# Optimization experiments

Hardware: AMD Instinct MI355X
Metric: run time of the kernel (lower is better)

Reference implementation:

```python
import jax, jax.numpy as jnp
import numpy as np

N_NODES = 64
N_EDGES = N_NODES * (N_NODES - 1)  # 4032 (fully connected, no self-loops)
BATCH = 64
N_IN = 64
N_HID = 128
N_OUT = 16


def _linear_params(key, fan_in, fan_out):
    # mimic torch nn.Linear default init: U(-1/sqrt(fan_in), 1/sqrt(fan_in))
    kw, kb = jax.random.split(key)
    s = 1.0 / np.sqrt(fan_in)
    W = jax.random.uniform(kw, (fan_in, fan_out), minval=-s, maxval=s, dtype=jnp.float32)
    b = jax.random.uniform(kb, (fan_out,), minval=-s, maxval=s, dtype=jnp.float32)
    return W, b


def setup_inputs() -> dict:
    key = jax.random.key(0)
    ks = jax.random.split(key, 10)
    # one-hot relation matrices for fully-connected graph without self loops
    pairs = np.array([(i, j) for i in range(N_NODES) for j in range(N_NODES) if i != j])
    eye = np.eye(N_NODES, dtype=np.float32)
    rel_send = jnp.asarray(eye[pairs[:, 0]])  # [E, N]
    rel_rec = jnp.asarray(eye[pairs[:, 1]])   # [E, N]

    x = jax.random.normal(ks[0], (BATCH, N_NODES, N_IN), dtype=jnp.float32)

    w1a, b1a = _linear_params(ks[1], N_IN, N_HID)
    w1b, b1b = _linear_params(ks[2], N_HID, N_HID)
    w2a, b2a = _linear_params(ks[3], 2 * N_HID, N_HID)
    w2b, b2b = _linear_params(ks[4], N_HID, N_HID)
    w3a, b3a = _linear_params(ks[5], N_HID, N_HID)
    w3b, b3b = _linear_params(ks[6], N_HID, N_HID)
    w4a, b4a = _linear_params(ks[7], 3 * N_HID, N_HID)  # factor=True
    w4b, b4b = _linear_params(ks[8], N_HID, N_HID)
    wout, bout = _linear_params(ks[9], N_HID, N_OUT)

    return dict(x=x, rel_rec=rel_rec, rel_send=rel_send,
                w1a=w1a, b1a=b1a, w1b=w1b, b1b=b1b,
                w2a=w2a, b2a=b2a, w2b=w2b, b2b=b2b,
                w3a=w3a, b3a=b3a, w3b=w3b, b3b=b3b,
                w4a=w4a, b4a=b4a, w4b=w4b, b4b=b4b,
                wout=wout, bout=bout)


def _mlp(x, wa, ba, wb, bb):
    # Linear -> ReLU -> Linear
    return jax.nn.relu(x @ wa + ba) @ wb + bb


def reference(x, rel_rec, rel_send,
              w1a, b1a, w1b, b1b,
              w2a, b2a, w2b, b2b,
              w3a, b3a, w3b, b3b,
              w4a, b4a, w4b, b4b,
              wout, bout):
    def node2edge(h):
        receivers = jnp.einsum('en,bnh->beh', rel_rec, h)
        senders = jnp.einsum('en,bnh->beh', rel_send, h)
        return jnp.concatenate([senders, receivers], axis=-1)  # [B,E,2H]

    def edge2node(e):
        agg = jnp.einsum('en,beh->bnh', rel_rec, e)
        norm = rel_rec.sum(0)[None, :, None]  # [1,N,1]
        return agg / (norm + 1e-6)

    h = _mlp(x, w1a, b1a, w1b, b1b)            # [B,N,H]
    e = _mlp(node2edge(h), w2a, b2a, w2b, b2b)  # [B,E,H]
    x_skip = e
    # factor=True branch
    n = _mlp(edge2node(e), w3a, b3a, w3b, b3b)  # [B,N,H]
    e2 = node2edge(n)                           # [B,E,2H]
    e2 = jnp.concatenate([e2, x_skip], axis=2)  # [B,E,3H]
    e2 = _mlp(e2, w4a, b4a, w4b, b4b)           # [B,E,H]
    return e2 @ wout + bout                     # [B,E,n_out]
```

## Files before the change

### kernel.cpp

```cpp
#include <hip/hip_runtime.h>
#include <hip/hip_bf16.h>


#define DI __device__ __forceinline__

typedef short bf16x8 __attribute__((ext_vector_type(8)));
typedef float f32x4 __attribute__((ext_vector_type(4)));
typedef unsigned short u16;
typedef unsigned long long u64;

static constexpr int NN = 64, NE = 4032, H = 128;

DI u16 f2bf(float f) {
  union { float f; unsigned u; } v; v.f = f;
  unsigned u = v.u;
  return (u16)((u + 0x7fffu + ((u >> 16) & 1u)) >> 16);
}
DI unsigned pk2(float a, float b) {
  union { __hip_bfloat162 h; unsigned u; } c;
  c.h = __float22bfloat162_rn(float2{a, b});
  return c.u;
}
DI f32x4 mf(bf16x8 a, bf16x8 b, f32x4 c) {
  return __builtin_amdgcn_mfma_f32_16x16x32_bf16(a, b, c, 0, 0, 0);
}
DI bf16x8 ldfrag(const u16* __restrict__ p, int idx, int l) {
  return *reinterpret_cast<const bf16x8*>(p + (idx * 64 + l) * 8);
}

__global__ __launch_bounds__(64) void prepack_kernel(
    const float* __restrict__ w1a, const float* __restrict__ w1b,
    const float* __restrict__ w2a, const float* __restrict__ w2b,
    const float* __restrict__ w3a, const float* __restrict__ w3b,
    const float* __restrict__ w4a, const float* __restrict__ w4b,
    const float* __restrict__ wout,
    const float* __restrict__ b2b, const float* __restrict__ b4b,
    const float* __restrict__ bout,
    u16* __restrict__ pk, float* __restrict__ c2, float* __restrict__ c4) {
  int seg = blockIdx.y, f = blockIdx.x, l = threadIdx.x;
  int h = l >> 4, mm = l & 15;
  if (seg == 10) {
    if (f >= 4) return;
    union { u16 u[8]; uint4 q; } o;
#pragma unroll
    for (int jj = 0; jj < 8; jj++) {
      int row = f * 32 + h * 8 + jj;
      float s0 = 0.f, s1 = 0.f, s2 = 0.f, s3 = 0.f;
      for (int j = 0; j < 128; j += 4) {
        s0 += w4b[row * 128 + j]     * wout[j * 16 + mm];
        s1 += w4b[row * 128 + j + 1] * wout[(j + 1) * 16 + mm];
        s2 += w4b[row * 128 + j + 2] * wout[(j + 2) * 16 + mm];
        s3 += w4b[row * 128 + j + 3] * wout[(j + 3) * 16 + mm];
      }
      o.u[jj] = f2bf((s0 + s1) + (s2 + s3));
    }
    *reinterpret_cast<uint4*>(pk + ((304 + f) * 64 + l) * 8) = o.q;
    return;
  }
  if (seg == 11) {
    if (f < 2) {
      int o = f * 64 + l;
      float s0 = 0.f, s1 = 0.f;
      for (int k = 0; k < 128; k += 2) {
        s0 += b2b[k] * w4a[(256 + k) * 128 + o];
        s1 += b2b[k + 1] * w4a[(256 + k + 1) * 128 + o];
      }
      c2[o] = s0 + s1;
    } else if (f == 2 && l < 16) {
      float s = bout[l];
      for (int k = 0; k < 128; k++) s += b4b[k] * wout[k * 16 + l];
      c4[l] = s;
    }
    return;
  }
  const float* src; int foff, nfrag, roff, pi;
  switch (seg) {
    case 0:  src = w1a; foff = 0;   nfrag = 16; roff = 0;   pi = 0; break;
    case 1:  src = w1b; foff = 16;  nfrag = 32; roff = 0;   pi = 1; break;
    case 2:  src = w2a; foff = 48;  nfrag = 32; roff = 0;   pi = 1; break;
    case 3:  src = w2a; foff = 80;  nfrag = 32; roff = 128; pi = 1; break;
    case 4:  src = w2b; foff = 112; nfrag = 32; roff = 0;   pi = 0; break;
    case 5:  src = w3a; foff = 144; nfrag = 32; roff = 0;   pi = 1; break;
    case 6:  src = w3b; foff = 176; nfrag = 32; roff = 0;   pi = 1; break;
    case 7:  src = w4a; foff = 208; nfrag = 32; roff = 0;   pi = 1; break;
    case 8:  src = w4a; foff = 240; nfrag = 32; roff = 128; pi = 1; break;
    default: src = w4a; foff = 272; nfrag = 32; roff = 256; pi = 0; break;
  }
  if (f >= nfrag) return;
  int kt = f >> 3, ct = f & 7;
  union { u16 u[8]; uint4 q; } o;
#pragma unroll
  for (int jj = 0; jj < 8; jj++) {
    int row = pi ? (kt * 32 + (jj >> 2) * 16 + h * 4 + (jj & 3))
                 : (kt * 32 + h * 8 + jj);
    o.u[jj] = f2bf(src[(roff + row) * 128 + ct * 16 + mm]);
  }
  *reinterpret_cast<uint4*>(pk + ((foff + f) * 64 + l) * 8) = o.q;
}

__global__ __launch_bounds__(512, 2) void node_kernel(
    const float* __restrict__ x, const u16* __restrict__ pk,
    const float* __restrict__ b1a, const float* __restrict__ b1b,
    const float* __restrict__ b2a,
    float* __restrict__ sproj, float* __restrict__ rproj) {
  __shared__ bf16x8 act[2][4][64];
  int blk = blockIdx.x, b = blk >> 2, nq = blk & 3;
  int tid = threadIdx.x, l = tid & 63, w = tid >> 6;
  int m = l & 15, h = l >> 4;
  int node = nq * 16 + m;
  const f32x4 Z = {0.f, 0.f, 0.f, 0.f};
  bf16x8 wpre[14];
  wpre[0] = ldfrag(pk, w, l);
  wpre[1] = ldfrag(pk, 8 + w, l);
#pragma unroll
  for (int kt = 0; kt < 4; kt++) {
    wpre[2 + kt]  = ldfrag(pk + 16 * 512, kt * 8 + w, l);
    wpre[6 + kt]  = ldfrag(pk + 48 * 512, kt * 8 + w, l);
    wpre[10 + kt] = ldfrag(pk + 80 * 512, kt * 8 + w, l);
  }
  f32x4 acc;
  {
    const float* xb = x + (b * NN + node) * 64;
    bf16x8 xin[2];
#pragma unroll
    for (int kt = 0; kt < 2; kt++) {
      f32x4 a0 = *(const f32x4*)(xb + kt * 32 + h * 8);
      f32x4 a1 = *(const f32x4*)(xb + kt * 32 + h * 8 + 4);
      union { unsigned u[4]; bf16x8 v; } t;
      t.u[0] = pk2(a0[0], a0[1]); t.u[1] = pk2(a0[2], a0[3]);
      t.u[2] = pk2(a1[0], a1[1]); t.u[3] = pk2(a1[2], a1[3]);
      xin[kt] = t.v;
    }
    acc = mf(wpre[0], xin[0], Z);
    acc = mf(wpre[1], xin[1], acc);
    f32x4 bb = *(const f32x4*)(b1a + w * 16 + h * 4);
    union { unsigned u[2]; u64 d; } p;
    p.u[0] = pk2(fmaxf(acc[0] + bb[0], 0.f), fmaxf(acc[1] + bb[1], 0.f));
    p.u[1] = pk2(fmaxf(acc[2] + bb[2], 0.f), fmaxf(acc[3] + bb[3], 0.f));
    reinterpret_cast<u64*>(&act[0][w >> 1][l])[w & 1] = p.d;
  }
  __syncthreads();
  bf16x8 ef[4];
#pragma unroll
  for (int kt = 0; kt < 4; kt++) ef[kt] = act[0][kt][l];
#pragma unroll
  for (int kt = 0; kt < 4; kt++)
    acc = mf(wpre[2 + kt], ef[kt], kt == 0 ? Z : acc);
  {
    f32x4 bb = *(const f32x4*)(b1b + w * 16 + h * 4);
    union { unsigned u[2]; u64 d; } p;
    p.u[0] = pk2(acc[0] + bb[0], acc[1] + bb[1]);
    p.u[1] = pk2(acc[2] + bb[2], acc[3] + bb[3]);
    reinterpret_cast<u64*>(&act[1][w >> 1][l])[w & 1] = p.d;
  }
  __syncthreads();
#pragma unroll
  for (int kt = 0; kt < 4; kt++) ef[kt] = act[1][kt][l];
#pragma unroll
  for (int kt = 0; kt < 4; kt++)
    acc = mf(wpre[6 + kt], ef[kt], kt == 0 ? Z : acc);
  *reinterpret_cast<f32x4*>(sproj + (b * NN + node) * H + w * 16 + h * 4) = acc;
#pragma unroll
  for (int kt = 0; kt < 4; kt++)
    acc = mf(wpre[10 + kt], ef[kt], kt == 0 ? Z : acc);
  {
    f32x4 bb = *(const f32x4*)(b2a + w * 16 + h * 4);
    f32x4 o = acc;
    o[0] += bb[0]; o[1] += bb[1]; o[2] += bb[2]; o[3] += bb[3];
    *reinterpret_cast<f32x4*>(rproj + (b * NN + node) * H + w * 16 + h * 4) = o;
  }
}

__global__ __launch_bounds__(512, 2) void agg_kernel(
    const float* __restrict__ sproj, const float* __restrict__ rproj,
    const u16* __restrict__ pk,
    const float* __restrict__ b2b, const float* __restrict__ b3a,
    const float* __restrict__ b3b, const float* __restrict__ b4a,
    const float* __restrict__ c2,
    float* __restrict__ s4, float* __restrict__ r4) {
  __shared__ f32x4 lred[8][8][64];
  __shared__ bf16x8 act[2][4][64];
  int blk = blockIdx.x, b = blk >> 2, jq = blk & 3;
  int tid = threadIdx.x, l = tid & 63, w = tid >> 6, m = l & 15, h = l >> 4;
  int j = jq * 16 + m;
  const float* rpb = rproj + (b * NN + j) * H;
  f32x4 rpv[8], accS[8];
#pragma unroll
  for (int k = 0; k < 8; k++) {
    rpv[k] = *(const f32x4*)(rpb + (k >> 1) * 32 + h * 8 + (k & 1) * 4);
    accS[k] = f32x4{0.f, 0.f, 0.f, 0.f};
  }
  const float* spb = sproj + b * NN * H;
  for (int i = w * 8; i < w * 8 + 8; i++) {
    const float* sp = spb + i * H;
#pragma unroll
    for (int k = 0; k < 8; k++) {
      f32x4 s = *(const f32x4*)(sp + (k >> 1) * 32 + h * 8 + (k & 1) * 4);
      f32x4 t = s + rpv[k];
      t[0] = fmaxf(t[0], 0.f); t[1] = fmaxf(t[1], 0.f);
      t[2] = fmaxf(t[2], 0.f); t[3] = fmaxf(t[3], 0.f);
      accS[k] += t;
    }
  }
  if ((j >> 3) == w) {
    const float* sp = spb + j * H;
#pragma unroll
    for (int k = 0; k < 8; k++) {
      f32x4 s = *(const f32x4*)(sp + (k >> 1) * 32 + h * 8 + (k & 1) * 4);
      f32x4 t = s + rpv[k];
      accS[k][0] -= fmaxf(t[0], 0.f); accS[k][1] -= fmaxf(t[1], 0.f);
      accS[k][2] -= fmaxf(t[2], 0.f); accS[k][3] -= fmaxf(t[3], 0.f);
    }
  }
#pragma unroll
  for (int k = 0; k < 8; k++) lred[w][k][l] = accS[k];
  bf16x8 wpre[20];
#pragma unroll
  for (int kt = 0; kt < 4; kt++) {
    wpre[kt]      = ldfrag(pk + 112 * 512, kt * 8 + w, l);
    wpre[4 + kt]  = ldfrag(pk + 144 * 512, kt * 8 + w, l);
    wpre[8 + kt]  = ldfrag(pk + 176 * 512, kt * 8 + w, l);
    wpre[12 + kt] = ldfrag(pk + 208 * 512, kt * 8 + w, l);
    wpre[16 + kt] = ldfrag(pk + 240 * 512, kt * 8 + w, l);
  }
  __syncthreads();
  if (w < 4) {
    f32x4 s0 = f32x4{0.f, 0.f, 0.f, 0.f}, s1 = s0;
#pragma unroll
    for (int ww = 0; ww < 8; ww++) {
      s0 += lred[ww][2 * w][l];
      s1 += lred[ww][2 * w + 1][l];
    }
    union { unsigned u[4]; bf16x8 v; } t;
    t.u[0] = pk2(s0[0], s0[1]); t.u[1] = pk2(s0[2], s0[3]);
    t.u[2] = pk2(s1[0], s1[1]); t.u[3] = pk2(s1[2], s1[3]);
    act[0][w][l] = t.v;
  }
  __syncthreads();
  const f32x4 Z = {0.f, 0.f, 0.f, 0.f};
  f32x4 acc;
  bf16x8 ef[4];
#pragma unroll
  for (int kt = 0; kt < 4; kt++) ef[kt] = act[0][kt][l];
#pragma unroll
  for (int kt = 0; kt < 4; kt++)
    acc = mf(wpre[kt], ef[kt], kt == 0 ? Z : acc);
  {
    const float inv = 1.0f / (63.0f + 1e-6f);
    const float binv = 63.0f * inv;
    f32x4 bb = *(const f32x4*)(b2b + w * 16 + h * 4);
    union { unsigned u[2]; u64 d; } p;
    p.u[0] = pk2(acc[0] * inv + bb[0] * binv, acc[1] * inv + bb[1] * binv);
    p.u[1] = pk2(acc[2] * inv + bb[2] * binv, acc[3] * inv + bb[3] * binv);
    reinterpret_cast<u64*>(&act[1][w >> 1][l])[w & 1] = p.d;
  }
  __syncthreads();
#pragma unroll
  for (int kt = 0; kt < 4; kt++) ef[kt] = act[1][kt][l];
#pragma unroll
  for (int kt = 0; kt < 4; kt++)
    acc = mf(wpre[4 + kt], ef[kt], kt == 0 ? Z : acc);
  {
    f32x4 bb = *(const f32x4*)(b3a + w * 16 + h * 4);
    union { unsigned u[2]; u64 d; } p;
    p.u[0] = pk2(fmaxf(acc[0] + bb[0], 0.f), fmaxf(acc[1] + bb[1], 0.f));
    p.u[1] = pk2(fmaxf(acc[2] + bb[2], 0.f), fmaxf(acc[3] + bb[3], 0.f));
    reinterpret_cast<u64*>(&act[0][w >> 1][l])[w & 1] = p.d;
  }
  __syncthreads();
#pragma unroll
  for (int kt = 0; kt < 4; kt++) ef[kt] = act[0][kt][l];
#pragma unroll
  for (int kt = 0; kt < 4; kt++)
    acc = mf(wpre[8 + kt], ef[kt], kt == 0 ? Z : acc);
  {
    f32x4 bb = *(const f32x4*)(b3b + w * 16 + h * 4);
    union { unsigned u[2]; u64 d; } p;
    p.u[0] = pk2(acc[0] + bb[0], acc[1] + bb[1]);
    p.u[1] = pk2(acc[2] + bb[2], acc[3] + bb[3]);
    reinterpret_cast<u64*>(&act[1][w >> 1][l])[w & 1] = p.d;
  }
  __syncthreads();
#pragma unroll
  for (int kt = 0; kt < 4; kt++) ef[kt] = act[1][kt][l];
#pragma unroll
  for (int kt = 0; kt < 4; kt++)
    acc = mf(wpre[12 + kt], ef[kt], kt == 0 ? Z : acc);
  {
    f32x4 cc = *(const f32x4*)(c2 + w * 16 + h * 4);
    f32x4 o = acc;
    o[0] += cc[0]; o[1] += cc[1]; o[2] += cc[2]; o[3] += cc[3];
    *reinterpret_cast<f32x4*>(s4 + (b * NN + j) * H + w * 16 + h * 4) = o;
  }
#pragma unroll
  for (int kt = 0; kt < 4; kt++)
    acc = mf(wpre[16 + kt], ef[kt], kt == 0 ? Z : acc);
  {
    f32x4 bb = *(const f32x4*)(b4a + w * 16 + h * 4);
    f32x4 o = acc;
    o[0] += bb[0]; o[1] += bb[1]; o[2] += bb[2]; o[3] += bb[3];
    *reinterpret_cast<f32x4*>(r4 + (b * NN + j) * H + w * 16 + h * 4) = o;
  }
}

__global__ __launch_bounds__(256, 4) void edge_kernel(
    const float* __restrict__ sproj, const float* __restrict__ rproj,
    const float* __restrict__ s4, const float* __restrict__ r4,
    const u16* __restrict__ pk, const float* __restrict__ c4,
    float* __restrict__ out) {
  __shared__ alignas(16) u16 bufA[8192];
  __shared__ alignas(16) u16 bufB[8192];
  int blk = blockIdx.x;
  int wg = (blk & 7) * 512 + (blk >> 3);
  int b = wg >> 6, i = wg & 63;
  int tid = threadIdx.x, l = tid & 63, w = tid >> 6;
  int m16 = l & 15, h = l >> 4;
  const f32x4 Z = {0.f, 0.f, 0.f, 0.f};
  int jnv[4];
#pragma unroll
  for (int n = 0; n < 4; n++) {
    int e = n * 16 + m16;
    int v = e + (e >= i ? 1 : 0); jnv[n] = v > 63 ? 63 : v;
  }
  bf16x8 wfv[4];
#pragma unroll
  for (int kt = 0; kt < 4; kt++) wfv[kt] = ldfrag(pk + 304 * 512, kt, l);
  f32x4 c4v = *(const f32x4*)(c4 + h * 4);
  {
    const float* spp = sproj + (b * NN + i) * H + w * 32 + h * 8;
    f32x4 s0 = *(const f32x4*)spp, s1 = *(const f32x4*)(spp + 4);
#pragma unroll
    for (int n = 0; n < 4; n++) {
      const float* rpp = rproj + (b * NN + jnv[n]) * H + w * 32 + h * 8;
      f32x4 r0 = *(const f32x4*)rpp, r1 = *(const f32x4*)(rpp + 4);
      union { unsigned u[4]; uint4 q; } t;
      t.u[0] = pk2(fmaxf(s0[0] + r0[0], 0.f), fmaxf(s0[1] + r0[1], 0.f));
      t.u[1] = pk2(fmaxf(s0[2] + r0[2], 0.f), fmaxf(s0[3] + r0[3], 0.f));
      t.u[2] = pk2(fmaxf(s1[0] + r1[0], 0.f), fmaxf(s1[1] + r1[1], 0.f));
      t.u[3] = pk2(fmaxf(s1[2] + r1[2], 0.f), fmaxf(s1[3] + r1[3], 0.f));
      *reinterpret_cast<uint4*>(&bufA[((w * 4 + n) * 64 + l) * 8]) = t.q;
    }
  }
  bf16x8 wv[8];
#pragma unroll
  for (int idx = 0; idx < 8; idx++)
    wv[idx] = ldfrag(pk + 112 * 512, (idx >> 1) * 8 + 2 * w + (idx & 1), l);
  __syncthreads();
  f32x4 acc[2][4];
  __builtin_amdgcn_s_setprio(1);
#pragma unroll
  for (int n = 0; n < 4; n++) {
    bf16x8 bf[4];
#pragma unroll
    for (int kt = 0; kt < 4; kt++)
      bf[kt] = *reinterpret_cast<const bf16x8*>(&bufA[((kt * 4 + n) * 64 + l) * 8]);
#pragma unroll
    for (int kt = 0; kt < 4; kt++)
#pragma unroll
      for (int m = 0; m < 2; m++)
        acc[m][n] = mf(wv[kt * 2 + m], bf[kt], kt == 0 ? Z : acc[m][n]);
  }
  __builtin_amdgcn_s_setprio(0);
#pragma unroll
  for (int idx = 0; idx < 8; idx++)
    wv[idx] = ldfrag(pk + 272 * 512, (idx >> 1) * 8 + 2 * w + (idx & 1), l);
  {
    int lane2b = (h >> 1) * 16 + m16;
    int jb = (h & 1) * 4;
#pragma unroll
    for (int m = 0; m < 2; m++)
#pragma unroll
      for (int n = 0; n < 4; n++) {
        union { unsigned u[2]; u64 d; } p;
        p.u[0] = pk2(acc[m][n][0], acc[m][n][1]);
        p.u[1] = pk2(acc[m][n][2], acc[m][n][3]);
        *reinterpret_cast<u64*>(
            &bufB[((w * 4 + n) * 64 + lane2b + m * 32) * 8 + jb]) = p.d;
      }
  }
  f32x4 s4v[2], rv[4][2];
#pragma unroll
  for (int m = 0; m < 2; m++)
    s4v[m] = *(const f32x4*)(s4 + (b * NN + i) * H + w * 32 + m * 16 + h * 4);
#pragma unroll
  for (int n = 0; n < 4; n++) {
    const float* r4p = r4 + (b * NN + jnv[n]) * H + w * 32 + h * 4;
#pragma unroll
    for (int m = 0; m < 2; m++) rv[n][m] = *(const f32x4*)(r4p + m * 16);
  }
  __syncthreads();
  __builtin_amdgcn_s_setprio(1);
#pragma unroll
  for (int n = 0; n < 4; n++) {
    bf16x8 bf[4];
#pragma unroll
    for (int kt = 0; kt < 4; kt++)
      bf[kt] = *reinterpret_cast<const bf16x8*>(&bufB[((kt * 4 + n) * 64 + l) * 8]);
#pragma unroll
    for (int kt = 0; kt < 4; kt++)
#pragma unroll
      for (int m = 0; m < 2; m++)
        acc[m][n] = mf(wv[kt * 2 + m], bf[kt], kt == 0 ? Z : acc[m][n]);
  }
  __builtin_amdgcn_s_setprio(0);
  {
    int lane2b = (h >> 1) * 16 + m16;
    int jb = (h & 1) * 4;
#pragma unroll
    for (int n = 0; n < 4; n++)
#pragma unroll
      for (int m = 0; m < 2; m++) {
        f32x4 r = rv[n][m];
        union { unsigned u[2]; u64 d; } p;
        p.u[0] = pk2(fmaxf(acc[m][n][0] + s4v[m][0] + r[0], 0.f),
                     fmaxf(acc[m][n][1] + s4v[m][1] + r[1], 0.f));
        p.u[1] = pk2(fmaxf(acc[m][n][2] + s4v[m][2] + r[2], 0.f),
                     fmaxf(acc[m][n][3] + s4v[m][3] + r[3], 0.f));
        *reinterpret_cast<u64*>(
            &bufA[((w * 4 + n) * 64 + lane2b + m * 32) * 8 + jb]) = p.d;
      }
  }
  __syncthreads();
  {
    bf16x8 bf[4];
#pragma unroll
    for (int kt = 0; kt < 4; kt++)
      bf[kt] = *reinterpret_cast<const bf16x8*>(&bufA[((kt * 4 + w) * 64 + l) * 8]);
    f32x4 a4 = Z;
#pragma unroll
    for (int kt = 0; kt < 4; kt++) a4 = mf(wfv[kt], bf[kt], a4);
    int jj = w * 16 + m16;
    if (jj < 63) {
      f32x4 o;
      o[0] = a4[0] + c4v[0]; o[1] = a4[1] + c4v[1];
      o[2] = a4[2] + c4v[2]; o[3] = a4[3] + c4v[3];
      *reinterpret_cast<f32x4*>(out + (b * NE + i * 63 + jj) * 16 + h * 4) = o;
    }
  }
}

extern "C" void kernel_launch(void* const* d_in, const int* in_sizes, int n_in,
                              void* d_out, int out_size, void* d_ws, size_t ws_size,
                              hipStream_t stream) {
  const float* x    = (const float*)d_in[0];
  const float* w1a  = (const float*)d_in[3];
  const float* b1a  = (const float*)d_in[4];
  const float* w1b  = (const float*)d_in[5];
  const float* b1b  = (const float*)d_in[6];
  const float* w2a  = (const float*)d_in[7];
  const float* b2a  = (const float*)d_in[8];
  const float* w2b  = (const float*)d_in[9];
  const float* b2b  = (const float*)d_in[10];
  const float* w3a  = (const float*)d_in[11];
  const float* b3a  = (const float*)d_in[12];
  const float* w3b  = (const float*)d_in[13];
  const float* b3b  = (const float*)d_in[14];
  const float* w4a  = (const float*)d_in[15];
  const float* b4a  = (const float*)d_in[16];
  const float* w4b  = (const float*)d_in[17];
  const float* b4b  = (const float*)d_in[18];
  const float* wout = (const float*)d_in[19];
  const float* bout = (const float*)d_in[20];
  float* out = (float*)d_out;

  float* sproj = (float*)d_ws;
  float* rproj = sproj + 524288;
  float* s4    = rproj + 524288;
  float* r4    = s4 + 524288;
  u16* pkw     = (u16*)(r4 + 524288);
  float* c2    = (float*)(pkw + 174080);
  float* c4    = c2 + 128;

  prepack_kernel<<<dim3(32, 12), 64, 0, stream>>>(
      w1a, w1b, w2a, w2b, w3a, w3b, w4a, w4b, wout, b2b, b4b, bout, pkw, c2, c4);
  node_kernel<<<256, 512, 0, stream>>>(x, pkw, b1a, b1b, b2a, sproj, rproj);
  agg_kernel<<<256, 512, 0, stream>>>(sproj, rproj, pkw, b2b, b3a, b3b, b4a, c2, s4, r4);
  edge_kernel<<<4096, 256, 0, stream>>>(sproj, rproj, s4, r4, pkw, c4, out);
}
```

Measured before the change: 94.77 us.

## Split edge kernel work across 8 waves per block instead of 4

```diff
diff --git a/kernel.cpp b/kernel.cpp
--- a/kernel.cpp
+++ b/kernel.cpp
@@ -303,7 +303,7 @@
   }
 }
 
-__global__ __launch_bounds__(256, 4) void edge_kernel(
+__global__ __launch_bounds__(512, 6) void edge_kernel(
     const float* __restrict__ sproj, const float* __restrict__ rproj,
     const float* __restrict__ s4, const float* __restrict__ r4,
     const u16* __restrict__ pk, const float* __restrict__ c4,
@@ -313,128 +313,97 @@
   int blk = blockIdx.x;
   int wg = (blk & 7) * 512 + (blk >> 3);
   int b = wg >> 6, i = wg & 63;
-  int tid = threadIdx.x, l = tid & 63, w = tid >> 6;
+  int tid = threadIdx.x, l = tid & 63, w8 = tid >> 6;
+  int n = w8 & 3, fh = w8 >> 2;
   int m16 = l & 15, h = l >> 4;
   const f32x4 Z = {0.f, 0.f, 0.f, 0.f};
-  int jnv[4];
-#pragma unroll
-  for (int n = 0; n < 4; n++) {
-    int e = n * 16 + m16;
-    int v = e + (e >= i ? 1 : 0); jnv[n] = v > 63 ? 63 : v;
-  }
-  bf16x8 wfv[4];
-#pragma unroll
-  for (int kt = 0; kt < 4; kt++) wfv[kt] = ldfrag(pk + 304 * 512, kt, l);
-  f32x4 c4v = *(const f32x4*)(c4 + h * 4);
-  {
-    const float* spp = sproj + (b * NN + i) * H + w * 32 + h * 8;
-    f32x4 s0 = *(const f32x4*)spp, s1 = *(const f32x4*)(spp + 4);
-#pragma unroll
-    for (int n = 0; n < 4; n++) {
-      const float* rpp = rproj + (b * NN + jnv[n]) * H + w * 32 + h * 8;
-      f32x4 r0 = *(const f32x4*)rpp, r1 = *(const f32x4*)(rpp + 4);
+  int e = n * 16 + m16;
+  int jn = e + (e >= i ? 1 : 0); if (jn > 63) jn = 63;
+  {
+    const float* sp = sproj + (b * NN + i) * H;
+    const float* rp = rproj + (b * NN + jn) * H;
+#pragma unroll
+    for (int kk = 0; kk < 2; kk++) {
+      int kt = fh * 2 + kk;
+      int k0 = kt * 32 + h * 8;
+      f32x4 s0 = *(const f32x4*)(sp + k0), s1 = *(const f32x4*)(sp + k0 + 4);
+      f32x4 r0 = *(const f32x4*)(rp + k0), r1 = *(const f32x4*)(rp + k0 + 4);
       union { unsigned u[4]; uint4 q; } t;
       t.u[0] = pk2(fmaxf(s0[0] + r0[0], 0.f), fmaxf(s0[1] + r0[1], 0.f));
       t.u[1] = pk2(fmaxf(s0[2] + r0[2], 0.f), fmaxf(s0[3] + r0[3], 0.f));
       t.u[2] = pk2(fmaxf(s1[0] + r1[0], 0.f), fmaxf(s1[1] + r1[1], 0.f));
       t.u[3] = pk2(fmaxf(s1[2] + r1[2], 0.f), fmaxf(s1[3] + r1[3], 0.f));
-      *reinterpret_cast<uint4*>(&bufA[((w * 4 + n) * 64 + l) * 8]) = t.q;
-    }
-  }
-  bf16x8 wv[8];
-#pragma unroll
-  for (int idx = 0; idx < 8; idx++)
-    wv[idx] = ldfrag(pk + 112 * 512, (idx >> 1) * 8 + 2 * w + (idx & 1), l);
-  __syncthreads();
-  f32x4 acc[2][4];
+      *reinterpret_cast<uint4*>(&bufA[((kt * 4 + n) * 64 + l) * 8]) = t.q;
+    }
+  }
+  __syncthreads();
+  f32x4 acc[4];
   __builtin_amdgcn_s_setprio(1);
 #pragma unroll
-  for (int n = 0; n < 4; n++) {
-    bf16x8 bf[4];
-#pragma unroll
-    for (int kt = 0; kt < 4; kt++)
-      bf[kt] = *reinterpret_cast<const bf16x8*>(&bufA[((kt * 4 + n) * 64 + l) * 8]);
-#pragma unroll
-    for (int kt = 0; kt < 4; kt++)
-#pragma unroll
-      for (int m = 0; m < 2; m++)
-        acc[m][n] = mf(wv[kt * 2 + m], bf[kt], kt == 0 ? Z : acc[m][n]);
+  for (int kt = 0; kt < 4; kt++) {
+    bf16x8 bf = *reinterpret_cast<const bf16x8*>(&bufA[((kt * 4 + n) * 64 + l) * 8]);
+#pragma unroll
+    for (int c = 0; c < 4; c++) {
+      bf16x8 wv = ldfrag(pk + 112 * 512, kt * 8 + fh * 4 + c, l);
+      acc[c] = mf(wv, bf, kt == 0 ? Z : acc[c]);
+    }
   }
   __builtin_amdgcn_s_setprio(0);
 #pragma unroll
-  for (int idx = 0; idx < 8; idx++)
-    wv[idx] = ldfrag(pk + 272 * 512, (idx >> 1) * 8 + 2 * w + (idx & 1), l);
-  {
-    int lane2b = (h >> 1) * 16 + m16;
-    int jb = (h & 1) * 4;
-#pragma unroll
-    for (int m = 0; m < 2; m++)
-#pragma unroll
-      for (int n = 0; n < 4; n++) {
-        union { unsigned u[2]; u64 d; } p;
-        p.u[0] = pk2(acc[m][n][0], acc[m][n][1]);
-        p.u[1] = pk2(acc[m][n][2], acc[m][n][3]);
-        *reinterpret_cast<u64*>(
-            &bufB[((w * 4 + n) * 64 + lane2b + m * 32) * 8 + jb]) = p.d;
-      }
-  }
-  f32x4 s4v[2], rv[4][2];
-#pragma unroll
-  for (int m = 0; m < 2; m++)
-    s4v[m] = *(const f32x4*)(s4 + (b * NN + i) * H + w * 32 + m * 16 + h * 4);
-#pragma unroll
-  for (int n = 0; n < 4; n++) {
-    const float* r4p = r4 + (b * NN + jnv[n]) * H + w * 32 + h * 4;
-#pragma unroll
-    for (int m = 0; m < 2; m++) rv[n][m] = *(const f32x4*)(r4p + m * 16);
+  for (int c = 0; c < 4; c++) {
+    int cg = fh * 4 + c;
+    int row = (cg >> 1) * 4 + n;
+    int h2 = (cg & 1) * 2 + (h >> 1);
+    union { unsigned u[2]; u64 d; } p;
+    p.u[0] = pk2(acc[c][0], acc[c][1]);
+    p.u[1] = pk2(acc[c][2], acc[c][3]);
+    *reinterpret_cast<u64*>(&bufB[(row * 64 + h2 * 16 + m16) * 8 + (h & 1) * 4]) = p.d;
   }
   __syncthreads();
   __builtin_amdgcn_s_setprio(1);
 #pragma unroll
-  for (int n = 0; n < 4; n++) {
-    bf16x8 bf[4];
-#pragma unroll
-    for (int kt = 0; kt < 4; kt++)
-      bf[kt] = *reinterpret_cast<const bf16x8*>(&bufB[((kt * 4 + n) * 64 + l) * 8]);
-#pragma unroll
-    for (int kt = 0; kt < 4; kt++)
-#pragma unroll
-      for (int m = 0; m < 2; m++)
-        acc[m][n] = mf(wv[kt * 2 + m], bf[kt], kt == 0 ? Z : acc[m][n]);
+  for (int kt = 0; kt < 4; kt++) {
+    bf16x8 bf = *reinterpret_cast<const bf16x8*>(&bufB[((kt * 4 + n) * 64 + l) * 8]);
+#pragma unroll
+    for (int c = 0; c < 4; c++) {
+      bf16x8 wv = ldfrag(pk + 272 * 512, kt * 8 + fh * 4 + c, l);
+      acc[c] = mf(wv, bf, kt == 0 ? Z : acc[c]);
+    }
   }
   __builtin_amdgcn_s_setprio(0);
   {
-    int lane2b = (h >> 1) * 16 + m16;
-    int jb = (h & 1) * 4;
-#pragma unroll
-    for (int n = 0; n < 4; n++)
-#pragma unroll
-      for (int m = 0; m < 2; m++) {
-        f32x4 r = rv[n][m];
-        union { unsigned u[2]; u64 d; } p;
-        p.u[0] = pk2(fmaxf(acc[m][n][0] + s4v[m][0] + r[0], 0.f),
-                     fmaxf(acc[m][n][1] + s4v[m][1] + r[1], 0.f));
-        p.u[1] = pk2(fmaxf(acc[m][n][2] + s4v[m][2] + r[2], 0.f),
-                     fmaxf(acc[m][n][3] + s4v[m][3] + r[3], 0.f));
-        *reinterpret_cast<u64*>(
-            &bufA[((w * 4 + n) * 64 + lane2b + m * 32) * 8 + jb]) = p.d;
-      }
-  }
-  __syncthreads();
-  {
-    bf16x8 bf[4];
-#pragma unroll
-    for (int kt = 0; kt < 4; kt++)
-      bf[kt] = *reinterpret_cast<const bf16x8*>(&bufA[((kt * 4 + w) * 64 + l) * 8]);
+    const float* s4p = s4 + (b * NN + i) * H + h * 4;
+    const float* r4p = r4 + (b * NN + jn) * H + h * 4;
+#pragma unroll
+    for (int c = 0; c < 4; c++) {
+      int cg = fh * 4 + c;
+      f32x4 sv = *(const f32x4*)(s4p + cg * 16);
+      f32x4 rv = *(const f32x4*)(r4p + cg * 16);
+      int row = (cg >> 1) * 4 + n;
+      int h2 = (cg & 1) * 2 + (h >> 1);
+      union { unsigned u[2]; u64 d; } p;
+      p.u[0] = pk2(fmaxf(acc[c][0] + sv[0] + rv[0], 0.f),
+                   fmaxf(acc[c][1] + sv[1] + rv[1], 0.f));
+      p.u[1] = pk2(fmaxf(acc[c][2] + sv[2] + rv[2], 0.f),
+                   fmaxf(acc[c][3] + sv[3] + rv[3], 0.f));
+      *reinterpret_cast<u64*>(&bufA[(row * 64 + h2 * 16 + m16) * 8 + (h & 1) * 4]) = p.d;
+    }
+  }
+  __syncthreads();
+  if (fh == 0) {
     f32x4 a4 = Z;
 #pragma unroll
-    for (int kt = 0; kt < 4; kt++) a4 = mf(wfv[kt], bf[kt], a4);
-    int jj = w * 16 + m16;
-    if (jj < 63) {
+    for (int kt = 0; kt < 4; kt++) {
+      bf16x8 bf = *reinterpret_cast<const bf16x8*>(&bufA[((kt * 4 + n) * 64 + l) * 8]);
+      bf16x8 wv = ldfrag(pk + 304 * 512, kt, l);
+      a4 = mf(wv, bf, a4);
+    }
+    if (e < 63) {
+      f32x4 c4v = *(const f32x4*)(c4 + h * 4);
       f32x4 o;
       o[0] = a4[0] + c4v[0]; o[1] = a4[1] + c4v[1];
       o[2] = a4[2] + c4v[2]; o[3] = a4[3] + c4v[3];
-      *reinterpret_cast<f32x4*>(out + (b * NE + i * 63 + jj) * 16 + h * 4) = o;
+      *reinterpret_cast<f32x4*>(out + (b * NE + i * 63 + e) * 16 + h * 4) = o;
     }
   }
 }
@@ -475,5 +444,5 @@
       w1a, w1b, w2a, w2b, w3a, w3b, w4a, w4b, wout, b2b, b4b, bout, pkw, c2, c4);
   node_kernel<<<256, 512, 0, stream>>>(x, pkw, b1a, b1b, b2a, sproj, rproj);
   agg_kernel<<<256, 512, 0, stream>>>(sproj, rproj, pkw, b2b, b3a, b3b, b4a, c2, s4, r4);
-  edge_kernel<<<4096, 256, 0, stream>>>(sproj, rproj, s4, r4, pkw, c4, out);
-}
+  edge_kernel<<<4096, 512, 0, stream>>>(sproj, rproj, s4, r4, pkw, c4, out);
+}
```

New measurement: 117.5 us. 1.24x slower.
